# Performance work log

Measured on AMD Instinct MI355X. Metric: run time of the kernel, lower is better.

## Reference

```python
import jax, jax.numpy as jnp
import numpy as np

B, C, H, W = 4, 64, 64, 64


def setup_inputs() -> dict:
    key = jax.random.key(0)
    ks = jax.random.split(key, 9)
    s = 1.0 / np.sqrt(C)
    return {
        "x1": jax.random.normal(ks[0], (B, C, H, W), dtype=jnp.float32),
        "x2": jax.random.normal(ks[1], (B, C, H, W), dtype=jnp.float32),
        "wq": jax.random.normal(ks[2], (C, C), dtype=jnp.float32) * s,
        "bq": jax.random.normal(ks[3], (C,), dtype=jnp.float32) * 0.01,
        "wk": jax.random.normal(ks[4], (C, C), dtype=jnp.float32) * s,
        "bk": jax.random.normal(ks[5], (C,), dtype=jnp.float32) * 0.01,
        "wv": jax.random.normal(ks[6], (C, C), dtype=jnp.float32) * s,
        "bv": jax.random.normal(ks[7], (C,), dtype=jnp.float32) * 0.01,
        "gamma": jax.random.normal(ks[8], (1,), dtype=jnp.float32) * 0.1,
    }


def _conv1x1(x, w, b):
    # 1x1 conv == per-pixel GEMM: [B,C,H,W] x [Cout,Cin] -> [B,Cout,H,W]
    return jnp.einsum('bchw,oc->bohw', x, w) + b[None, :, None, None]


def reference(x1, x2, wq, bq, wk, bk, wv, bv, gamma):
    b, c, h, w = x1.shape
    n = h * w
    q = _conv1x1(x1, wq, bq).reshape(b, c, n)   # [B,C,N]
    k = _conv1x1(x2, wk, bk).reshape(b, c, n)   # [B,C,N]
    v = _conv1x1(x2, wv, bv).reshape(b, c, n)   # [B,C,N]
    # attention[b,i,j] = sum_c q[b,c,i] * k[b,c,j]  -> [B,N,N]
    attn = jnp.einsum('bci,bcj->bij', q, k)
    attn = jax.nn.softmax(attn, axis=-1)
    # out[b,c,i] = sum_j v[b,c,j] * attn[b,i,j]
    out = jnp.einsum('bcj,bij->bci', v, attn).reshape(b, c, h, w)
    return gamma[0] * out + x1
```

## Files before the change

kernel.cpp:

```cpp
#include <hip/hip_runtime.h>
#include <cstdint>
#include <cstddef>


typedef __bf16 bf16x4 __attribute__((ext_vector_type(4)));
typedef __bf16 bf16x8 __attribute__((ext_vector_type(8)));
typedef float  f32x4  __attribute__((ext_vector_type(4)));
typedef float  f32x16 __attribute__((ext_vector_type(16)));
typedef short  s16x4  __attribute__((ext_vector_type(4)));

constexpr int C = 64;
constexpr int N = 4096;
constexpr float LOG2E = 1.44269504088896340736f;

static __device__ __forceinline__ f32x4 mfma16(bf16x8 a, bf16x8 b, f32x4 c) {
    return __builtin_amdgcn_mfma_f32_16x16x32_bf16(a, b, c, 0, 0, 0);
}
static __device__ __forceinline__ f32x16 mfma32(bf16x8 a, bf16x8 b, f32x16 c) {
    return __builtin_amdgcn_mfma_f32_32x32x16_bf16(a, b, c, 0, 0, 0);
}
static __device__ __forceinline__ f32x16 pv_mfma(bf16x4 a, bf16x4 b, f32x16 c) {
#if __has_builtin(__builtin_amdgcn_mfma_f32_32x32x8bf16_1k)
    union U { bf16x4 h; s16x4 s; };
    U ua; ua.h = a;
    U ub; ub.h = b;
    return __builtin_amdgcn_mfma_f32_32x32x8bf16_1k(ua.s, ub.s, c, 0, 0, 0);
#else
    const __bf16 z = (__bf16)0.0f;
    bf16x8 a8 = {a[0], a[1], a[2], a[3], z, z, z, z};
    bf16x8 b8 = {b[0], b[1], b[2], b[3], z, z, z, z};
    return __builtin_amdgcn_mfma_f32_32x32x16_bf16(a8, b8, c, 0, 0, 0);
#endif
}
static __device__ __forceinline__ float fast_exp2(float x) {
#if __has_builtin(__builtin_amdgcn_exp2f)
    return __builtin_amdgcn_exp2f(x);
#else
    return exp2f(x);
#endif
}

__global__ __launch_bounds__(256) void qkv_kernel(
    const float* __restrict__ x1, const float* __restrict__ x2,
    const float* __restrict__ wq, const float* __restrict__ bq,
    const float* __restrict__ wk, const float* __restrict__ bk,
    const float* __restrict__ wv, const float* __restrict__ bv,
    __bf16* __restrict__ qo, __bf16* __restrict__ ko, __bf16* __restrict__ vo)
{
    __shared__ __bf16 wl[64][72];
    __shared__ __bf16 tout[64][72];

    const int bid  = blockIdx.x;
    const int kind = bid >> 8;
    const int pg   = bid & 255;
    const int b     = pg >> 6;
    const int nbase = (pg & 63) * 64;
    const int tid   = threadIdx.x;

    const float* wsel = kind == 0 ? wq : (kind == 1 ? wk : wv);
    const float* bsel = kind == 0 ? bq : (kind == 1 ? bk : bv);
    const float* xsel = kind == 0 ? x1 : x2;
    __bf16*      osel = kind == 0 ? qo : (kind == 1 ? ko : vo);

#pragma unroll
    for (int i = 0; i < 4; ++i) {
        int idx = i * 256 + tid;
        int row = idx >> 4, c4 = (idx & 15) * 4;
        float4 a = *(const float4*)(wsel + row * 64 + c4);
        bf16x4 h = {(__bf16)a.x, (__bf16)a.y, (__bf16)a.z, (__bf16)a.w};
        *(bf16x4*)&wl[row][c4] = h;
    }
    __syncthreads();

    const int wave = tid >> 6, lane = tid & 63;
    const int l = lane & 15, qd = lane >> 4;
    const int p = nbase + wave * 16 + l;

    const float* xb = xsel + (size_t)b * C * N + p;
    bf16x8 ax[2];
#pragma unroll
    for (int ks = 0; ks < 2; ++ks)
#pragma unroll
        for (int j = 0; j < 8; ++j)
            ax[ks][j] = (__bf16)xb[(size_t)(ks * 32 + qd * 8 + j) * N];

    if (kind < 2) {
        const float scale = kind == 0 ? LOG2E : 1.0f;
#pragma unroll
        for (int ot = 0; ot < 4; ++ot) {
            const float bb = bsel[ot * 16 + l];
            f32x4 acc = {bb, bb, bb, bb};
#pragma unroll
            for (int ks = 0; ks < 2; ++ks) {
                bf16x8 bw = *(const bf16x8*)&wl[ot * 16 + l][ks * 32 + qd * 8];
                acc = mfma16(ax[ks], bw, acc);
            }
#pragma unroll
            for (int r = 0; r < 4; ++r) {
                int px = wave * 16 + qd * 4 + r;
                tout[px][ot * 16 + l] = (__bf16)(acc[r] * scale);
            }
        }
        __syncthreads();

        const int tile = tid >> 7, t7 = tid & 127;
        const int kc = t7 >> 5, h2 = (t7 >> 4) & 1, ilp = (t7 & 15) * 2;
        const size_t tb = ((size_t)b * 128 + (nbase >> 5) + tile) * 2048;
        const size_t off = tb + kc * 512 + h2 * 256 + ilp * 8;
        bf16x8 ra = *(const bf16x8*)&tout[tile * 32 + ilp][kc * 16 + h2 * 8];
        bf16x8 rb = *(const bf16x8*)&tout[tile * 32 + ilp + 1][kc * 16 + h2 * 8];
        *(bf16x8*)&osel[off]     = ra;
        *(bf16x8*)&osel[off + 8] = rb;
    } else {
#pragma unroll
        for (int ct = 0; ct < 4; ++ct) {
            f32x4 acc;
#pragma unroll
            for (int r = 0; r < 4; ++r) acc[r] = bsel[ct * 16 + qd * 4 + r];
#pragma unroll
            for (int ks = 0; ks < 2; ++ks) {
                bf16x8 aw = *(const bf16x8*)&wl[ct * 16 + l][ks * 32 + qd * 8];
                acc = mfma16(aw, ax[ks], acc);
            }
            bf16x4 pk = {(__bf16)acc[0], (__bf16)acc[1], (__bf16)acc[2], (__bf16)acc[3]};
            *(bf16x4*)&tout[wave * 16 + l][ct * 16 + qd * 4] = pk;
        }
        __syncthreads();

        const int tile = tid >> 7, t7 = tid & 127;
        const int g = t7 >> 5, vh = (t7 >> 4) & 1, c0 = (t7 & 15) * 4;
        const int pxb = tile * 32 + g * 8 + vh * 4;
        bf16x4 e0 = *(const bf16x4*)&tout[pxb + 0][c0];
        bf16x4 e1 = *(const bf16x4*)&tout[pxb + 1][c0];
        bf16x4 e2 = *(const bf16x4*)&tout[pxb + 2][c0];
        bf16x4 e3 = *(const bf16x4*)&tout[pxb + 3][c0];
        bf16x8 o1, o2;
        o1[0]=e0[0]; o1[1]=e1[0]; o1[2]=e2[0]; o1[3]=e3[0];
        o1[4]=e0[1]; o1[5]=e1[1]; o1[6]=e2[1]; o1[7]=e3[1];
        o2[0]=e0[2]; o2[1]=e1[2]; o2[2]=e2[2]; o2[3]=e3[2];
        o2[4]=e0[3]; o2[5]=e1[3]; o2[6]=e2[3]; o2[7]=e3[3];
        const size_t tb = ((size_t)b * 128 + (nbase >> 5) + tile) * 2048;
        const size_t off = tb + g * 512 + vh * 256 + c0 * 4;
        *(bf16x8*)&osel[off]     = o1;
        *(bf16x8*)&osel[off + 8] = o2;
    }
}

__global__ __launch_bounds__(512, 2) void attn_kernel(
    const __bf16* __restrict__ qg, const __bf16* __restrict__ kg,
    const __bf16* __restrict__ vg, const float* __restrict__ x1,
    const float* __restrict__ gamma, float* __restrict__ out)
{
    __shared__ float lds_acc[3][64][64];
    __shared__ float lds_l[8][64];

    const int bid = blockIdx.x;
    const int xcd = bid & 7;
    const int b   = xcd >> 1;
    const int rt  = ((bid >> 3) << 1) | (xcd & 1);
    const int ibase = rt * 64;

    const int tid  = threadIdx.x;
    const int wave = tid >> 6, lane = tid & 63;
    const int il = lane & 31, hi = lane >> 5;

    const __bf16* qt = qg + ((size_t)b * 128 + rt * 2) * 2048;
    const __bf16* kt = kg + (size_t)b * 128 * 2048 + (size_t)(wave * 16) * 2048;
    const __bf16* vt = vg + (size_t)b * 128 * 2048 + (size_t)(wave * 16) * 2048;

    bf16x8 bqf[2][4];
#pragma unroll
    for (int qs = 0; qs < 2; ++qs)
#pragma unroll
        for (int kc = 0; kc < 4; ++kc)
            bqf[qs][kc] = *(const bf16x8*)(qt + qs * 2048 + kc * 512 + lane * 8);

    f32x16 accO[4];
#pragma unroll
    for (int a = 0; a < 4; ++a)
#pragma unroll
        for (int r = 0; r < 16; ++r) accO[a][r] = 0.f;
    float lsum[2] = {0.f, 0.f};

    bf16x8 akf[2][4];
    bf16x4 avf[2][4];

#pragma unroll
    for (int kc = 0; kc < 4; ++kc)
        akf[0][kc] = *(const bf16x8*)(kt + kc * 512 + lane * 8);

#pragma unroll 2
    for (int t = 0; t < 16; ++t) {
        const int cur = t & 1;
        if (t < 15) {
#pragma unroll
            for (int kc = 0; kc < 4; ++kc)
                akf[cur ^ 1][kc] = *(const bf16x8*)(kt + (size_t)(t + 1) * 2048 + kc * 512 + lane * 8);
        }
#pragma unroll
        for (int ct = 0; ct < 2; ++ct)
#pragma unroll
            for (int kcs = 0; kcs < 4; ++kcs)
                avf[ct][kcs] = *(const bf16x4*)(vt + (size_t)t * 2048 + kcs * 512 + hi * 256 + ct * 128 + il * 4);

#pragma unroll
        for (int qs = 0; qs < 2; ++qs) {
            f32x16 st;
#pragma unroll
            for (int r = 0; r < 16; ++r) st[r] = 0.f;
#pragma unroll
            for (int kc = 0; kc < 4; ++kc) st = mfma32(akf[cur][kc], bqf[qs][kc], st);

            bf16x4 bp[4];
            float lp0 = 0.f, lp1 = 0.f, lp2 = 0.f, lp3 = 0.f;
#pragma unroll
            for (int g = 0; g < 4; ++g) {
                float p0 = fast_exp2(st[g * 4 + 0]);
                float p1 = fast_exp2(st[g * 4 + 1]);
                float p2 = fast_exp2(st[g * 4 + 2]);
                float p3 = fast_exp2(st[g * 4 + 3]);
                lp0 += p0; lp1 += p1; lp2 += p2; lp3 += p3;
                bp[g][0] = (__bf16)p0; bp[g][1] = (__bf16)p1;
                bp[g][2] = (__bf16)p2; bp[g][3] = (__bf16)p3;
            }
            lsum[qs] += (lp0 + lp1) + (lp2 + lp3);

#pragma unroll
            for (int ct = 0; ct < 2; ++ct)
#pragma unroll
                for (int g = 0; g < 4; ++g)
                    accO[qs * 2 + ct] = pv_mfma(avf[ct][g], bp[g], accO[qs * 2 + ct]);
        }
    }

#pragma unroll
    for (int qs = 0; qs < 2; ++qs) lsum[qs] += __shfl_xor(lsum[qs], 32);
    if (hi == 0) {
        lds_l[wave][il]      = lsum[0];
        lds_l[wave][32 + il] = lsum[1];
    }

#define ACC_STORE(SLOT)                                                        \
    do {                                                                       \
        _Pragma("unroll")                                                      \
        for (int qs = 0; qs < 2; ++qs)                                         \
            _Pragma("unroll")                                                  \
            for (int ct = 0; ct < 2; ++ct)                                     \
                _Pragma("unroll")                                              \
                for (int r = 0; r < 16; ++r)                                   \
                    lds_acc[SLOT][ct * 32 + (r & 3) + 8 * (r >> 2) + 4 * hi][qs * 32 + il] = accO[qs * 2 + ct][r]; \
    } while (0)
#define ACC_LOAD(SLOT)                                                         \
    do {                                                                       \
        _Pragma("unroll")                                                      \
        for (int qs = 0; qs < 2; ++qs)                                         \
            _Pragma("unroll")                                                  \
            for (int ct = 0; ct < 2; ++ct)                                     \
                _Pragma("unroll")                                              \
                for (int r = 0; r < 16; ++r)                                   \
                    accO[qs * 2 + ct][r] += lds_acc[SLOT][ct * 32 + (r & 3) + 8 * (r >> 2) + 4 * hi][qs * 32 + il]; \
    } while (0)

    if (wave >= 5) ACC_STORE(wave - 5);
    __syncthreads();
    if (wave >= 1 && wave <= 3) ACC_LOAD(wave - 1);
    __syncthreads();
    if (wave >= 2 && wave <= 4) ACC_STORE(wave - 2);
    __syncthreads();
    if (wave <= 1) ACC_LOAD(wave);
    if (wave == 0) ACC_LOAD(2);
    __syncthreads();
    if (wave == 1) ACC_STORE(0);
    __syncthreads();
    if (wave == 0) { ACC_LOAD(0); ACC_STORE(0); }
    __syncthreads();
#undef ACC_STORE
#undef ACC_LOAD

    const float g = gamma[0];
    {
        const int c  = tid >> 3;
        const int i8 = (tid & 7) * 8;
        float lv[8];
#pragma unroll
        for (int e = 0; e < 8; ++e) {
            float s = 0.f;
#pragma unroll
            for (int w = 0; w < 8; ++w) s += lds_l[w][i8 + e];
            lv[e] = s;
        }
        const size_t idx = ((size_t)b * C + c) * N + ibase + i8;
        f32x4 o0 = *(const f32x4*)&lds_acc[0][c][i8];
        f32x4 o1 = *(const f32x4*)&lds_acc[0][c][i8 + 4];
        f32x4 x0 = *(const f32x4*)(x1 + idx);
        f32x4 x4 = *(const f32x4*)(x1 + idx + 4);
        f32x4 r0, r1;
#pragma unroll
        for (int e = 0; e < 4; ++e) {
            r0[e] = g * o0[e] / lv[e] + x0[e];
            r1[e] = g * o1[e] / lv[4 + e] + x4[e];
        }
        *(f32x4*)(out + idx) = r0;
        *(f32x4*)(out + idx + 4) = r1;
    }
}

extern "C" void kernel_launch(void* const* d_in, const int* in_sizes, int n_in,
                              void* d_out, int out_size, void* d_ws, size_t ws_size,
                              hipStream_t stream) {
    const float* x1    = (const float*)d_in[0];
    const float* x2    = (const float*)d_in[1];
    const float* wq    = (const float*)d_in[2];
    const float* bqv   = (const float*)d_in[3];
    const float* wk    = (const float*)d_in[4];
    const float* bkv   = (const float*)d_in[5];
    const float* wv    = (const float*)d_in[6];
    const float* bvv   = (const float*)d_in[7];
    const float* gamma = (const float*)d_in[8];
    float* out = (float*)d_out;

    __bf16* qws = (__bf16*)d_ws;
    __bf16* kws = qws + (size_t)4 * 128 * 2048;
    __bf16* vws = kws + (size_t)4 * 128 * 2048;

    qkv_kernel<<<768, 256, 0, stream>>>(x1, x2, wq, bqv, wk, bkv, wv, bvv, qws, kws, vws);
    attn_kernel<<<256, 512, 0, stream>>>(qws, kws, vws, x1, gamma, out);
}
```

Before: 102.2 us.

## Halve query tile per block to double grid and raise occupancy

The attention kernel now processes 32 query rows per block instead of 64, doubling the grid to 512 blocks and raising launch bounds to 4 blocks per CU. Per-wave register state (accumulators, Q fragments) halves, and V is loaded as 8-wide vectors split into two 4-wide MFMA operands, which required a matching change to the V layout written by the QKV kernel. The K/V register double-buffering prefetch is removed in favour of relying on more resident waves for latency hiding. In exchange, each block reloads all of K and V for fewer queries, doubling K/V read traffic from cache.

```diff
diff --git a/kernel.cpp b/kernel.cpp
--- a/kernel.cpp
+++ b/kernel.cpp
@@ -3,6 +3,7 @@
 #include <cstddef>
 
 
+typedef __bf16 bf16x2 __attribute__((ext_vector_type(2)));
 typedef __bf16 bf16x4 __attribute__((ext_vector_type(4)));
 typedef __bf16 bf16x8 __attribute__((ext_vector_type(8)));
 typedef float  f32x4  __attribute__((ext_vector_type(4)));
@@ -128,137 +129,115 @@
         __syncthreads();
 
         const int tile = tid >> 7, t7 = tid & 127;
-        const int g = t7 >> 5, vh = (t7 >> 4) & 1, c0 = (t7 & 15) * 4;
+        const int g = t7 >> 5, vh = (t7 >> 4) & 1, il0 = (t7 & 15) * 2;
         const int pxb = tile * 32 + g * 8 + vh * 4;
-        bf16x4 e0 = *(const bf16x4*)&tout[pxb + 0][c0];
-        bf16x4 e1 = *(const bf16x4*)&tout[pxb + 1][c0];
-        bf16x4 e2 = *(const bf16x4*)&tout[pxb + 2][c0];
-        bf16x4 e3 = *(const bf16x4*)&tout[pxb + 3][c0];
-        bf16x8 o1, o2;
-        o1[0]=e0[0]; o1[1]=e1[0]; o1[2]=e2[0]; o1[3]=e3[0];
-        o1[4]=e0[1]; o1[5]=e1[1]; o1[6]=e2[1]; o1[7]=e3[1];
-        o2[0]=e0[2]; o2[1]=e1[2]; o2[2]=e2[2]; o2[3]=e3[2];
-        o2[4]=e0[3]; o2[5]=e1[3]; o2[6]=e2[3]; o2[7]=e3[3];
+        bf16x8 oA, oB;
+#pragma unroll
+        for (int ct = 0; ct < 2; ++ct)
+#pragma unroll
+            for (int e = 0; e < 4; ++e) {
+                bf16x2 pr = *(const bf16x2*)&tout[pxb + e][ct * 32 + il0];
+                oA[ct * 4 + e] = pr[0];
+                oB[ct * 4 + e] = pr[1];
+            }
         const size_t tb = ((size_t)b * 128 + (nbase >> 5) + tile) * 2048;
-        const size_t off = tb + g * 512 + vh * 256 + c0 * 4;
-        *(bf16x8*)&osel[off]     = o1;
-        *(bf16x8*)&osel[off + 8] = o2;
+        const size_t off = tb + g * 512 + vh * 256 + il0 * 8;
+        *(bf16x8*)&osel[off]     = oA;
+        *(bf16x8*)&osel[off + 8] = oB;
     }
 }
 
-__global__ __launch_bounds__(512, 2) void attn_kernel(
+__global__ __launch_bounds__(512, 4) void attn_kernel(
     const __bf16* __restrict__ qg, const __bf16* __restrict__ kg,
     const __bf16* __restrict__ vg, const float* __restrict__ x1,
     const float* __restrict__ gamma, float* __restrict__ out)
 {
-    __shared__ float lds_acc[3][64][64];
-    __shared__ float lds_l[8][64];
+    __shared__ float lds_acc[3][64][32];
+    __shared__ float lds_l[8][32];
 
     const int bid = blockIdx.x;
     const int xcd = bid & 7;
     const int b   = xcd >> 1;
     const int rt  = ((bid >> 3) << 1) | (xcd & 1);
-    const int ibase = rt * 64;
+    const int ibase = rt * 32;
 
     const int tid  = threadIdx.x;
     const int wave = tid >> 6, lane = tid & 63;
     const int il = lane & 31, hi = lane >> 5;
 
-    const __bf16* qt = qg + ((size_t)b * 128 + rt * 2) * 2048;
+    const __bf16* qt = qg + ((size_t)b * 128 + rt) * 2048;
     const __bf16* kt = kg + (size_t)b * 128 * 2048 + (size_t)(wave * 16) * 2048;
     const __bf16* vt = vg + (size_t)b * 128 * 2048 + (size_t)(wave * 16) * 2048;
 
-    bf16x8 bqf[2][4];
-#pragma unroll
-    for (int qs = 0; qs < 2; ++qs)
+    bf16x8 bqf[4];
+#pragma unroll
+    for (int kc = 0; kc < 4; ++kc)
+        bqf[kc] = *(const bf16x8*)(qt + kc * 512 + lane * 8);
+
+    f32x16 accO[2];
+#pragma unroll
+    for (int a = 0; a < 2; ++a)
+#pragma unroll
+        for (int r = 0; r < 16; ++r) accO[a][r] = 0.f;
+    float lsum = 0.f;
+
+#pragma unroll 1
+    for (int t = 0; t < 16; ++t) {
+        bf16x8 ak[4], av[4];
 #pragma unroll
         for (int kc = 0; kc < 4; ++kc)
-            bqf[qs][kc] = *(const bf16x8*)(qt + qs * 2048 + kc * 512 + lane * 8);
-
-    f32x16 accO[4];
-#pragma unroll
-    for (int a = 0; a < 4; ++a)
-#pragma unroll
-        for (int r = 0; r < 16; ++r) accO[a][r] = 0.f;
-    float lsum[2] = {0.f, 0.f};
-
-    bf16x8 akf[2][4];
-    bf16x4 avf[2][4];
-
-#pragma unroll
-    for (int kc = 0; kc < 4; ++kc)
-        akf[0][kc] = *(const bf16x8*)(kt + kc * 512 + lane * 8);
-
-#pragma unroll 2
-    for (int t = 0; t < 16; ++t) {
-        const int cur = t & 1;
-        if (t < 15) {
-#pragma unroll
-            for (int kc = 0; kc < 4; ++kc)
-                akf[cur ^ 1][kc] = *(const bf16x8*)(kt + (size_t)(t + 1) * 2048 + kc * 512 + lane * 8);
-        }
-#pragma unroll
-        for (int ct = 0; ct < 2; ++ct)
-#pragma unroll
-            for (int kcs = 0; kcs < 4; ++kcs)
-                avf[ct][kcs] = *(const bf16x4*)(vt + (size_t)t * 2048 + kcs * 512 + hi * 256 + ct * 128 + il * 4);
-
-#pragma unroll
-        for (int qs = 0; qs < 2; ++qs) {
-            f32x16 st;
-#pragma unroll
-            for (int r = 0; r < 16; ++r) st[r] = 0.f;
-#pragma unroll
-            for (int kc = 0; kc < 4; ++kc) st = mfma32(akf[cur][kc], bqf[qs][kc], st);
-
-            bf16x4 bp[4];
-            float lp0 = 0.f, lp1 = 0.f, lp2 = 0.f, lp3 = 0.f;
-#pragma unroll
-            for (int g = 0; g < 4; ++g) {
-                float p0 = fast_exp2(st[g * 4 + 0]);
-                float p1 = fast_exp2(st[g * 4 + 1]);
-                float p2 = fast_exp2(st[g * 4 + 2]);
-                float p3 = fast_exp2(st[g * 4 + 3]);
-                lp0 += p0; lp1 += p1; lp2 += p2; lp3 += p3;
-                bp[g][0] = (__bf16)p0; bp[g][1] = (__bf16)p1;
-                bp[g][2] = (__bf16)p2; bp[g][3] = (__bf16)p3;
-            }
-            lsum[qs] += (lp0 + lp1) + (lp2 + lp3);
-
-#pragma unroll
-            for (int ct = 0; ct < 2; ++ct)
-#pragma unroll
-                for (int g = 0; g < 4; ++g)
-                    accO[qs * 2 + ct] = pv_mfma(avf[ct][g], bp[g], accO[qs * 2 + ct]);
+            ak[kc] = *(const bf16x8*)(kt + (size_t)t * 2048 + kc * 512 + lane * 8);
+#pragma unroll
+        for (int g = 0; g < 4; ++g)
+            av[g] = *(const bf16x8*)(vt + (size_t)t * 2048 + g * 512 + hi * 256 + il * 8);
+
+        f32x16 st;
+#pragma unroll
+        for (int r = 0; r < 16; ++r) st[r] = 0.f;
+#pragma unroll
+        for (int kc = 0; kc < 4; ++kc) st = mfma32(ak[kc], bqf[kc], st);
+
+        bf16x4 bp[4];
+        float lp0 = 0.f, lp1 = 0.f, lp2 = 0.f, lp3 = 0.f;
+#pragma unroll
+        for (int g = 0; g < 4; ++g) {
+            float p0 = fast_exp2(st[g * 4 + 0]);
+            float p1 = fast_exp2(st[g * 4 + 1]);
+            float p2 = fast_exp2(st[g * 4 + 2]);
+            float p3 = fast_exp2(st[g * 4 + 3]);
+            lp0 += p0; lp1 += p1; lp2 += p2; lp3 += p3;
+            bp[g][0] = (__bf16)p0; bp[g][1] = (__bf16)p1;
+            bp[g][2] = (__bf16)p2; bp[g][3] = (__bf16)p3;
+        }
+        lsum += (lp0 + lp1) + (lp2 + lp3);
+
+#pragma unroll
+        for (int g = 0; g < 4; ++g) {
+            bf16x4 v0 = __builtin_shufflevector(av[g], av[g], 0, 1, 2, 3);
+            bf16x4 v1 = __builtin_shufflevector(av[g], av[g], 4, 5, 6, 7);
+            accO[0] = pv_mfma(v0, bp[g], accO[0]);
+            accO[1] = pv_mfma(v1, bp[g], accO[1]);
         }
     }
 
-#pragma unroll
-    for (int qs = 0; qs < 2; ++qs) lsum[qs] += __shfl_xor(lsum[qs], 32);
-    if (hi == 0) {
-        lds_l[wave][il]      = lsum[0];
-        lds_l[wave][32 + il] = lsum[1];
-    }
+    lsum += __shfl_xor(lsum, 32);
+    if (hi == 0) lds_l[wave][il] = lsum;
 
 #define ACC_STORE(SLOT)                                                        \
     do {                                                                       \
         _Pragma("unroll")                                                      \
-        for (int qs = 0; qs < 2; ++qs)                                         \
+        for (int ct = 0; ct < 2; ++ct)                                         \
             _Pragma("unroll")                                                  \
-            for (int ct = 0; ct < 2; ++ct)                                     \
-                _Pragma("unroll")                                              \
-                for (int r = 0; r < 16; ++r)                                   \
-                    lds_acc[SLOT][ct * 32 + (r & 3) + 8 * (r >> 2) + 4 * hi][qs * 32 + il] = accO[qs * 2 + ct][r]; \
+            for (int r = 0; r < 16; ++r)                                       \
+                lds_acc[SLOT][ct * 32 + (r & 3) + 8 * (r >> 2) + 4 * hi][il] = accO[ct][r]; \
     } while (0)
 #define ACC_LOAD(SLOT)                                                         \
     do {                                                                       \
         _Pragma("unroll")                                                      \
-        for (int qs = 0; qs < 2; ++qs)                                         \
+        for (int ct = 0; ct < 2; ++ct)                                         \
             _Pragma("unroll")                                                  \
-            for (int ct = 0; ct < 2; ++ct)                                     \
-                _Pragma("unroll")                                              \
-                for (int r = 0; r < 16; ++r)                                   \
-                    accO[qs * 2 + ct][r] += lds_acc[SLOT][ct * 32 + (r & 3) + 8 * (r >> 2) + 4 * hi][qs * 32 + il]; \
+            for (int r = 0; r < 16; ++r)                                       \
+                accO[ct][r] += lds_acc[SLOT][ct * 32 + (r & 3) + 8 * (r >> 2) + 4 * hi][il]; \
     } while (0)
 
     if (wave >= 5) ACC_STORE(wave - 5);
@@ -280,28 +259,22 @@
     const float g = gamma[0];
     {
         const int c  = tid >> 3;
-        const int i8 = (tid & 7) * 8;
-        float lv[8];
-#pragma unroll
-        for (int e = 0; e < 8; ++e) {
-            float s = 0.f;
-#pragma unroll
-            for (int w = 0; w < 8; ++w) s += lds_l[w][i8 + e];
-            lv[e] = s;
-        }
-        const size_t idx = ((size_t)b * C + c) * N + ibase + i8;
-        f32x4 o0 = *(const f32x4*)&lds_acc[0][c][i8];
-        f32x4 o1 = *(const f32x4*)&lds_acc[0][c][i8 + 4];
+        const int i4 = (tid & 7) * 4;
+        f32x4 lv = {0.f, 0.f, 0.f, 0.f};
+#pragma unroll
+        for (int w = 0; w < 8; ++w) {
+            f32x4 lw = *(const f32x4*)&lds_l[w][i4];
+#pragma unroll
+            for (int e = 0; e < 4; ++e) lv[e] += lw[e];
+        }
+        const size_t idx = ((size_t)b * C + c) * N + ibase + i4;
+        f32x4 o0 = *(const f32x4*)&lds_acc[0][c][i4];
         f32x4 x0 = *(const f32x4*)(x1 + idx);
-        f32x4 x4 = *(const f32x4*)(x1 + idx + 4);
-        f32x4 r0, r1;
-#pragma unroll
-        for (int e = 0; e < 4; ++e) {
+        f32x4 r0;
+#pragma unroll
+        for (int e = 0; e < 4; ++e)
             r0[e] = g * o0[e] / lv[e] + x0[e];
-            r1[e] = g * o1[e] / lv[4 + e] + x4[e];
-        }
         *(f32x4*)(out + idx) = r0;
-        *(f32x4*)(out + idx + 4) = r1;
     }
 }
 
@@ -324,5 +297,5 @@
     __bf16* vws = kws + (size_t)4 * 128 * 2048;
 
     qkv_kernel<<<768, 256, 0, stream>>>(x1, x2, wq, bqv, wk, bkv, wv, bvv, qws, kws, vws);
-    attn_kernel<<<256, 512, 0, stream>>>(qws, kws, vws, x1, gamma, out);
-}
+    attn_kernel<<<512, 512, 0, stream>>>(qws, kws, vws, x1, gamma, out);
+}
```

Result: no change. 104.0 us (+1.8%).

## Use 32x32x16 MFMA for PV via permlane32 swap and relaid V

Applied to the files above, without the earlier changes.

Replaces the eight 32x32x8 MFMAs per PV tile with four 32x32x16 MFMAs. The probability registers are repacked into the K=16 operand layout with v_permlane32_swap, and the V tile layout written by the qkv kernel is changed so each lane loads contiguous bf16x8 operands. This halves the PV MFMA instruction count and uses wider V loads. In exchange it adds cross-lane swaps, and the qkv epilogue now does scalar LDS reads instead of vector ones.

```diff
diff --git a/kernel.cpp b/kernel.cpp
--- a/kernel.cpp
+++ b/kernel.cpp
@@ -3,11 +3,11 @@
 #include <cstddef>
 
 
+typedef __bf16 bf16x2 __attribute__((ext_vector_type(2)));
 typedef __bf16 bf16x4 __attribute__((ext_vector_type(4)));
 typedef __bf16 bf16x8 __attribute__((ext_vector_type(8)));
 typedef float  f32x4  __attribute__((ext_vector_type(4)));
 typedef float  f32x16 __attribute__((ext_vector_type(16)));
-typedef short  s16x4  __attribute__((ext_vector_type(4)));
 
 constexpr int C = 64;
 constexpr int N = 4096;
@@ -18,19 +18,6 @@
 }
 static __device__ __forceinline__ f32x16 mfma32(bf16x8 a, bf16x8 b, f32x16 c) {
     return __builtin_amdgcn_mfma_f32_32x32x16_bf16(a, b, c, 0, 0, 0);
-}
-static __device__ __forceinline__ f32x16 pv_mfma(bf16x4 a, bf16x4 b, f32x16 c) {
-#if __has_builtin(__builtin_amdgcn_mfma_f32_32x32x8bf16_1k)
-    union U { bf16x4 h; s16x4 s; };
-    U ua; ua.h = a;
-    U ub; ub.h = b;
-    return __builtin_amdgcn_mfma_f32_32x32x8bf16_1k(ua.s, ub.s, c, 0, 0, 0);
-#else
-    const __bf16 z = (__bf16)0.0f;
-    bf16x8 a8 = {a[0], a[1], a[2], a[3], z, z, z, z};
-    bf16x8 b8 = {b[0], b[1], b[2], b[3], z, z, z, z};
-    return __builtin_amdgcn_mfma_f32_32x32x16_bf16(a8, b8, c, 0, 0, 0);
-#endif
 }
 static __device__ __forceinline__ float fast_exp2(float x) {
 #if __has_builtin(__builtin_amdgcn_exp2f)
@@ -38,6 +25,11 @@
 #else
     return exp2f(x);
 #endif
+}
+static __device__ __forceinline__ uint32_t pack2(float a, float b) {
+    union { uint32_t u; bf16x2 h; } w;
+    w.h = bf16x2{(__bf16)a, (__bf16)b};
+    return w.u;
 }
 
 __global__ __launch_bounds__(256) void qkv_kernel(
@@ -128,21 +120,18 @@
         __syncthreads();
 
         const int tile = tid >> 7, t7 = tid & 127;
-        const int g = t7 >> 5, vh = (t7 >> 4) & 1, c0 = (t7 & 15) * 4;
-        const int pxb = tile * 32 + g * 8 + vh * 4;
-        bf16x4 e0 = *(const bf16x4*)&tout[pxb + 0][c0];
-        bf16x4 e1 = *(const bf16x4*)&tout[pxb + 1][c0];
-        bf16x4 e2 = *(const bf16x4*)&tout[pxb + 2][c0];
-        bf16x4 e3 = *(const bf16x4*)&tout[pxb + 3][c0];
-        bf16x8 o1, o2;
-        o1[0]=e0[0]; o1[1]=e1[0]; o1[2]=e2[0]; o1[3]=e3[0];
-        o1[4]=e0[1]; o1[5]=e1[1]; o1[6]=e2[1]; o1[7]=e3[1];
-        o2[0]=e0[2]; o2[1]=e1[2]; o2[2]=e2[2]; o2[3]=e3[2];
-        o2[4]=e0[3]; o2[5]=e1[3]; o2[6]=e2[3]; o2[7]=e3[3];
+        const int G = t7 >> 6, vh = (t7 >> 5) & 1, il = t7 & 31;
+        const int pxb = tile * 32 + G * 16 + vh * 8;
+        bf16x8 oA, oB;
+#pragma unroll
+        for (int e = 0; e < 8; ++e) {
+            oA[e] = tout[pxb + e][il];
+            oB[e] = tout[pxb + e][32 + il];
+        }
         const size_t tb = ((size_t)b * 128 + (nbase >> 5) + tile) * 2048;
-        const size_t off = tb + g * 512 + vh * 256 + c0 * 4;
-        *(bf16x8*)&osel[off]     = o1;
-        *(bf16x8*)&osel[off + 8] = o2;
+        const size_t off = tb + G * 1024 + vh * 512 + (size_t)il * 16;
+        *(bf16x8*)&osel[off]     = oA;
+        *(bf16x8*)&osel[off + 8] = oB;
     }
 }
 
@@ -183,7 +172,6 @@
     float lsum[2] = {0.f, 0.f};
 
     bf16x8 akf[2][4];
-    bf16x4 avf[2][4];
 
 #pragma unroll
     for (int kc = 0; kc < 4; ++kc)
@@ -197,11 +185,12 @@
             for (int kc = 0; kc < 4; ++kc)
                 akf[cur ^ 1][kc] = *(const bf16x8*)(kt + (size_t)(t + 1) * 2048 + kc * 512 + lane * 8);
         }
+        bf16x8 av[2][2];
 #pragma unroll
         for (int ct = 0; ct < 2; ++ct)
 #pragma unroll
-            for (int kcs = 0; kcs < 4; ++kcs)
-                avf[ct][kcs] = *(const bf16x4*)(vt + (size_t)t * 2048 + kcs * 512 + hi * 256 + ct * 128 + il * 4);
+            for (int G = 0; G < 2; ++G)
+                av[ct][G] = *(const bf16x8*)(vt + (size_t)t * 2048 + G * 1024 + hi * 512 + il * 16 + ct * 8);
 
 #pragma unroll
         for (int qs = 0; qs < 2; ++qs) {
@@ -211,25 +200,34 @@
 #pragma unroll
             for (int kc = 0; kc < 4; ++kc) st = mfma32(akf[cur][kc], bqf[qs][kc], st);
 
-            bf16x4 bp[4];
-            float lp0 = 0.f, lp1 = 0.f, lp2 = 0.f, lp3 = 0.f;
-#pragma unroll
-            for (int g = 0; g < 4; ++g) {
-                float p0 = fast_exp2(st[g * 4 + 0]);
-                float p1 = fast_exp2(st[g * 4 + 1]);
-                float p2 = fast_exp2(st[g * 4 + 2]);
-                float p3 = fast_exp2(st[g * 4 + 3]);
-                lp0 += p0; lp1 += p1; lp2 += p2; lp3 += p3;
-                bp[g][0] = (__bf16)p0; bp[g][1] = (__bf16)p1;
-                bp[g][2] = (__bf16)p2; bp[g][3] = (__bf16)p3;
-            }
-            lsum[qs] += (lp0 + lp1) + (lp2 + lp3);
-
-#pragma unroll
-            for (int ct = 0; ct < 2; ++ct)
-#pragma unroll
-                for (int g = 0; g < 4; ++g)
-                    accO[qs * 2 + ct] = pv_mfma(avf[ct][g], bp[g], accO[qs * 2 + ct]);
+            float p[16];
+            float lp0 = 0.f, lp1 = 0.f;
+#pragma unroll
+            for (int r = 0; r < 16; r += 2) {
+                p[r]     = fast_exp2(st[r]);
+                p[r + 1] = fast_exp2(st[r + 1]);
+                lp0 += p[r];
+                lp1 += p[r + 1];
+            }
+            lsum[qs] += lp0 + lp1;
+
+            uint32_t a0 = pack2(p[0],  p[1]),  a1 = pack2(p[2],  p[3]);
+            uint32_t b0 = pack2(p[4],  p[5]),  b1 = pack2(p[6],  p[7]);
+            uint32_t c0 = pack2(p[8],  p[9]),  c1 = pack2(p[10], p[11]);
+            uint32_t d0 = pack2(p[12], p[13]), d1 = pack2(p[14], p[15]);
+            asm("v_permlane32_swap_b32 %0, %1" : "+v"(a0), "+v"(b0));
+            asm("v_permlane32_swap_b32 %0, %1" : "+v"(a1), "+v"(b1));
+            asm("v_permlane32_swap_b32 %0, %1" : "+v"(c0), "+v"(d0));
+            asm("v_permlane32_swap_b32 %0, %1" : "+v"(c1), "+v"(d1));
+            union F { uint32_t u[4]; bf16x8 v; } f0, f1;
+            f0.u[0] = a0; f0.u[1] = a1; f0.u[2] = b0; f0.u[3] = b1;
+            f1.u[0] = c0; f1.u[1] = c1; f1.u[2] = d0; f1.u[3] = d1;
+
+#pragma unroll
+            for (int ct = 0; ct < 2; ++ct) {
+                accO[qs * 2 + ct] = mfma32(av[ct][0], f0.v, accO[qs * 2 + ct]);
+                accO[qs * 2 + ct] = mfma32(av[ct][1], f1.v, accO[qs * 2 + ct]);
+            }
         }
     }
 
```

Result: faster. 100.1 us (-2.0%).
